# Performance work log

Measured on AMD Instinct MI355X. Metric: run time of the kernel, lower is better.

Reference implementation:

```python
import jax, jax.numpy as jnp
import numpy as np

B, H, W, C, NH, WS, SS = 32, 56, 56, 128, 4, 7, 3
L = H * W
N = WS * WS
HD = C // NH
EPS = 1e-5


def _rel_pos_index():
    coords = np.stack(np.meshgrid(np.arange(WS), np.arange(WS), indexing='ij'))  # (2,ws,ws)
    flat = coords.reshape(2, -1)  # (2,N)
    rel = flat[:, :, None] - flat[:, None, :]  # (2,N,N)
    rel = rel.transpose(1, 2, 0).astype(np.int64)
    rel[..., 0] += WS - 1
    rel[..., 1] += WS - 1
    rel[..., 0] *= 2 * WS - 1
    return jnp.asarray(rel.sum(-1), dtype=jnp.int32)  # (N,N)


def setup_inputs() -> dict:
    key = jax.random.key(0)
    ks = jax.random.split(key, 8)
    s = 0.02
    return {
        'x': jax.random.normal(ks[0], (B, L, C), jnp.float32),
        'norm1_g': jnp.ones((C,), jnp.float32),
        'norm1_b': jnp.zeros((C,), jnp.float32),
        'qkv_w': jax.random.normal(ks[1], (3 * C, C), jnp.float32) * s,
        'qkv_b': jnp.zeros((3 * C,), jnp.float32),
        'rpb_table': jax.random.normal(ks[2], ((2 * WS - 1) ** 2, NH), jnp.float32) * s,
        'proj_w': jax.random.normal(ks[3], (C, C), jnp.float32) * s,
        'proj_b': jnp.zeros((C,), jnp.float32),
        'norm2_g': jnp.ones((C,), jnp.float32),
        'norm2_b': jnp.zeros((C,), jnp.float32),
        'fc1_w': jax.random.normal(ks[4], (4 * C, C), jnp.float32) * s,
        'fc1_b': jnp.zeros((4 * C,), jnp.float32),
        'fc2_w': jax.random.normal(ks[5], (C, 4 * C), jnp.float32) * s,
        'fc2_b': jnp.zeros((C,), jnp.float32),
        'rel_idx': _rel_pos_index(),
    }


def _ln(h, g, b):
    mu = jnp.mean(h, axis=-1, keepdims=True)
    var = jnp.mean((h - mu) ** 2, axis=-1, keepdims=True)
    return (h - mu) * jax.lax.rsqrt(var + EPS) * g + b


def reference(x, norm1_g, norm1_b, qkv_w, qkv_b, rpb_table, proj_w, proj_b,
              norm2_g, norm2_b, fc1_w, fc1_b, fc2_w, fc2_b, rel_idx):
    nHw, nWw = H // WS, W // WS
    scale = HD ** (-0.5)

    shortcut = x
    h = _ln(x, norm1_g, norm1_b).reshape(B, H, W, C)
    # cyclic shift
    h = jnp.roll(h, shift=(-SS, -SS), axis=(1, 2))
    # window partition -> (B*nW, N, C)
    w = h.reshape(B, nHw, WS, nWw, WS, C).transpose(0, 1, 3, 2, 4, 5)
    w = w.reshape(B * nHw * nWw, N, C)

    qkv = w @ qkv_w.T + qkv_b  # (Bw, N, 3C)
    q, k, v = jnp.split(qkv, 3, axis=-1)
    q = q.reshape(-1, N, NH, HD).transpose(0, 2, 1, 3)  # (Bw, nh, N, hd)
    k = k.reshape(-1, N, NH, HD).transpose(0, 2, 1, 3)
    v = v.reshape(-1, N, NH, HD).transpose(0, 2, 1, 3)

    attn = jnp.einsum('bhnd,bhmd->bhnm', q * scale, k)
    bias = rpb_table[rel_idx.reshape(-1)].reshape(N, N, NH).transpose(2, 0, 1)  # (nh,N,N)
    attn = jax.nn.softmax(attn + bias[None], axis=-1)

    out = jnp.einsum('bhnm,bhmd->bhnd', attn, v)
    out = out.transpose(0, 2, 1, 3).reshape(-1, N, C)
    out = out @ proj_w.T + proj_b

    # window reverse + un-shift
    out = out.reshape(B, nHw, nWw, WS, WS, C).transpose(0, 1, 3, 2, 4, 5)
    out = out.reshape(B, H, W, C)
    out = jnp.roll(out, shift=(SS, SS), axis=(1, 2)).reshape(B, L, C)

    x = shortcut + out
    h2 = _ln(x, norm2_g, norm2_b)
    mlp = jax.nn.gelu(h2 @ fc1_w.T + fc1_b, approximate=False) @ fc2_w.T + fc2_b
    return x + mlp
```

## Files before the change

kernel.cpp:

```cpp
#include <hip/hip_runtime.h>

typedef unsigned short ushort_t;
typedef unsigned int uint_t;

typedef __bf16 bf16x8 __attribute__((ext_vector_type(8)));
typedef float f32x4 __attribute__((ext_vector_type(4)));

static __device__ __forceinline__ float bf2f(ushort_t h) {
    return __uint_as_float(((uint_t)h) << 16);
}
static __device__ __forceinline__ ushort_t f2bf(float f) {
    uint_t u = __float_as_uint(f);
    u = u + 0x7FFFu + ((u >> 16) & 1u);
    return (ushort_t)(u >> 16);
}
static __device__ __forceinline__ uint_t pkbf(float lo, float hi) {
    uint_t a = __float_as_uint(lo) + 0x8000u;
    uint_t b = __float_as_uint(hi) + 0x8000u;
    return __builtin_amdgcn_perm(b, a, 0x07060302u);
}

#define BB 32
#define HH 56
#define WW_ 56
#define CC 128
#define NHEAD 4
#define WS 7
#define SS 3
#define LL (HH * WW_)
#define NTOK (BB * LL)
#define NWIN (BB * 64)
#define NN 49
#define HD 32
#define QKS 32
#define PLS 40
#define VTS 72

static __device__ __forceinline__ int win2tok(int wid) {
    int win = wid / NN, t = wid - win * NN;
    int bb = win >> 6, wrem = win & 63;
    int wi = wrem >> 3, wj = wrem & 7;
    int ti = t / WS, tj = t - ti * WS;
    int hh = wi * WS + ti + SS; if (hh >= HH) hh -= HH;
    int ww = wj * WS + tj + SS; if (ww >= WW_) ww -= WW_;
    return bb * LL + hh * WW_ + ww;
}

__global__ __launch_bounds__(256) void prep_weights(
    const float* __restrict__ qkv_w, const float* __restrict__ proj_w,
    const float* __restrict__ fc1_w, const float* __restrict__ fc2_w,
    ushort_t* __restrict__ dst) {
    int i = blockIdx.x * 256 + threadIdx.x;
    const float* src;
    int off;
    if (i < 49152)        { src = qkv_w;  off = i; }
    else if (i < 65536)   { src = proj_w; off = i - 49152; }
    else if (i < 131072)  { src = fc1_w;  off = i - 65536; }
    else                  { src = fc2_w;  off = i - 131072; }
    dst[i] = f2bf(src[off]);
}

__global__ __launch_bounds__(256) void build_bias(
    const float* __restrict__ rpb, const int* __restrict__ rel_idx,
    float* __restrict__ bias) {
    int h = blockIdx.x;
    for (int idx = threadIdx.x; idx < 4096; idx += 256) {
        int i = idx >> 6, j = idx & 63;
        float v = 0.f;
        if (i < NN && j < NN)
            v = rpb[(size_t)rel_idx[i * NN + j] * NHEAD + h];
        bias[h * 4096 + idx] = v;
    }
}

__global__ __launch_bounds__(256) void win_block(
    const float* __restrict__ x, const float* __restrict__ g1,
    const float* __restrict__ b1, const ushort_t* __restrict__ wq,
    const float* __restrict__ qkv_b, const float* __restrict__ bias,
    ushort_t* __restrict__ attn_out, int win0) {
    __shared__ __align__(16) ushort_t U[16384];
    __shared__ __align__(16) ushort_t HV[NHEAD][32 * VTS];
    const int tid = threadIdx.x;
    const int wave = tid >> 6;
    const int lane = tid & 63;
    const int l16 = lane & 15;
    const int quad = lane >> 4;
    const int h = wave;
    const int win = win0 + blockIdx.x;
    const float scale = 0.17677669529663687f;

    ushort_t* XLN = U;
    ushort_t* QL = U + h * 4096;
    ushort_t* KL = QL + 2048;
    ushort_t* PL = QL;
    ushort_t* VT = HV[h];

    {
        int row = tid >> 2;
        int ch0 = (tid & 3) * 32;
        int t = (row < NN) ? row : 0;
        int gtok = win2tok(win * NN + t);
        const float* xp = x + (size_t)gtok * CC + ch0;
        float v[32];
        float s = 0.f, sq = 0.f;
        #pragma unroll
        for (int i = 0; i < 4; ++i) {
            float4 a0 = *(const float4*)(xp + i * 8);
            float4 a1 = *(const float4*)(xp + i * 8 + 4);
            v[i * 8 + 0] = a0.x; v[i * 8 + 1] = a0.y;
            v[i * 8 + 2] = a0.z; v[i * 8 + 3] = a0.w;
            v[i * 8 + 4] = a1.x; v[i * 8 + 5] = a1.y;
            v[i * 8 + 6] = a1.z; v[i * 8 + 7] = a1.w;
            #pragma unroll
            for (int j = 0; j < 8; ++j) { s += v[i * 8 + j]; sq += v[i * 8 + j] * v[i * 8 + j]; }
        }
        s += __shfl_xor(s, 1);  sq += __shfl_xor(sq, 1);
        s += __shfl_xor(s, 2);  sq += __shfl_xor(sq, 2);
        float mean = s * (1.0f / 128.0f);
        float var = sq * (1.0f / 128.0f) - mean * mean;
        float rstd = rsqrtf(var + 1e-5f);
        #pragma unroll
        for (int i = 0; i < 4; ++i) {
            ushort_t tmp[8];
            #pragma unroll
            for (int j = 0; j < 8; ++j) {
                int c = ch0 + i * 8 + j;
                tmp[j] = f2bf((v[i * 8 + j] - mean) * rstd * g1[c] + b1[c]);
            }
            *(uint4*)&XLN[row * 136 + ch0 + i * 8] = *(const uint4*)tmp;
        }
    }
    __syncthreads();

    bf16x8 tf[4][4];
    #pragma unroll
    for (int kk = 0; kk < 4; ++kk)
        #pragma unroll
        for (int i = 0; i < 4; ++i)
            tf[kk][i] = *(const bf16x8*)&XLN[(16 * i + l16) * 136 + kk * 32 + quad * 8];
    __syncthreads();

    {
        f32x4 s1[2][4];
        #pragma unroll
        for (int j = 0; j < 2; ++j)
            #pragma unroll
            for (int i = 0; i < 4; ++i)
                s1[j][i] = (f32x4){0.f, 0.f, 0.f, 0.f};
        #pragma unroll
        for (int kk = 0; kk < 4; ++kk)
            #pragma unroll
            for (int j = 0; j < 2; ++j) {
                bf16x8 wf = *(const bf16x8*)&wq[(size_t)(h * 32 + 16 * j + l16) * 128 + kk * 32 + quad * 8];
                #pragma unroll
                for (int i = 0; i < 4; ++i)
                    s1[j][i] = __builtin_amdgcn_mfma_f32_16x16x32_bf16(wf, tf[kk][i], s1[j][i], 0, 0, 0);
            }
        #pragma unroll
        for (int j = 0; j < 2; ++j) {
            float4 bv = *(const float4*)&qkv_b[h * 32 + 16 * j + quad * 4];
            #pragma unroll
            for (int i = 0; i < 4; ++i) {
                uint2 pk;
                pk.x = pkbf((s1[j][i][0] + bv.x) * scale, (s1[j][i][1] + bv.y) * scale);
                pk.y = pkbf((s1[j][i][2] + bv.z) * scale, (s1[j][i][3] + bv.w) * scale);
                *(uint2*)&QL[(16 * i + l16) * QKS + 16 * j + quad * 4] = pk;
            }
        }
    }
    {
        f32x4 s1[2][4];
        #pragma unroll
        for (int j = 0; j < 2; ++j)
            #pragma unroll
            for (int i = 0; i < 4; ++i)
                s1[j][i] = (f32x4){0.f, 0.f, 0.f, 0.f};
        #pragma unroll
        for (int kk = 0; kk < 4; ++kk)
            #pragma unroll
            for (int j = 0; j < 2; ++j) {
                bf16x8 wf = *(const bf16x8*)&wq[(size_t)(128 + h * 32 + 16 * j + l16) * 128 + kk * 32 + quad * 8];
                #pragma unroll
                for (int i = 0; i < 4; ++i)
                    s1[j][i] = __builtin_amdgcn_mfma_f32_16x16x32_bf16(wf, tf[kk][i], s1[j][i], 0, 0, 0);
            }
        #pragma unroll
        for (int j = 0; j < 2; ++j) {
            float4 bv = *(const float4*)&qkv_b[128 + h * 32 + 16 * j + quad * 4];
            #pragma unroll
            for (int i = 0; i < 4; ++i) {
                uint2 pk;
                pk.x = pkbf(s1[j][i][0] + bv.x, s1[j][i][1] + bv.y);
                pk.y = pkbf(s1[j][i][2] + bv.z, s1[j][i][3] + bv.w);
                *(uint2*)&KL[(16 * i + l16) * QKS + 16 * j + quad * 4] = pk;
            }
        }
    }
    {
        f32x4 sv[4][2];
        #pragma unroll
        for (int i = 0; i < 4; ++i)
            #pragma unroll
            for (int j = 0; j < 2; ++j)
                sv[i][j] = (f32x4){0.f, 0.f, 0.f, 0.f};
        #pragma unroll
        for (int kk = 0; kk < 4; ++kk)
            #pragma unroll
            for (int j = 0; j < 2; ++j) {
                bf16x8 wf = *(const bf16x8*)&wq[(size_t)(256 + h * 32 + 16 * j + l16) * 128 + kk * 32 + quad * 8];
                #pragma unroll
                for (int i = 0; i < 4; ++i)
                    sv[i][j] = __builtin_amdgcn_mfma_f32_16x16x32_bf16(tf[kk][i], wf, sv[i][j], 0, 0, 0);
            }
        #pragma unroll
        for (int j = 0; j < 2; ++j) {
            float bvv = qkv_b[256 + h * 32 + 16 * j + l16];
            #pragma unroll
            for (int i = 0; i < 4; ++i) {
                uint2 pk;
                pk.x = pkbf(sv[i][j][0] + bvv, sv[i][j][1] + bvv);
                pk.y = pkbf(sv[i][j][2] + bvv, sv[i][j][3] + bvv);
                *(uint2*)&VT[(16 * j + l16) * VTS + 16 * i + quad * 4] = pk;
            }
        }
    }

    f32x4 s[4][4];
    {
        bf16x8 qa[4], kb[4];
        #pragma unroll
        for (int t = 0; t < 4; ++t) {
            qa[t] = *(const bf16x8*)&QL[(16 * t + l16) * QKS + quad * 8];
            kb[t] = *(const bf16x8*)&KL[(16 * t + l16) * QKS + quad * 8];
        }
        #pragma unroll
        for (int mi = 0; mi < 4; ++mi)
            #pragma unroll
            for (int ni = 0; ni < 4; ++ni) {
                f32x4 z = {0.f, 0.f, 0.f, 0.f};
                s[mi][ni] = __builtin_amdgcn_mfma_f32_16x16x32_bf16(qa[mi], kb[ni], z, 0, 0, 0);
            }
    }

    const float* bh = bias + h * 4096;
    #pragma unroll
    for (int mi = 0; mi < 4; ++mi)
        #pragma unroll
        for (int ni = 0; ni < 4; ++ni)
            #pragma unroll
            for (int r = 0; r < 4; ++r)
                s[mi][ni][r] += bh[(16 * mi + quad * 4 + r) * 64 + 16 * ni + l16];

    #pragma unroll
    for (int mi = 0; mi < 4; ++mi)
        #pragma unroll
        for (int r = 0; r < 4; ++r) {
            float m01 = fmaxf(s[mi][0][r], s[mi][1][r]);
            float m2 = s[mi][2][r];
            float m3 = (l16 == 0) ? s[mi][3][r] : -3.0e38f;
            float mx = fmaxf(fmaxf(m01, m2), m3);
            mx = fmaxf(mx, __shfl_xor(mx, 1));
            mx = fmaxf(mx, __shfl_xor(mx, 2));
            mx = fmaxf(mx, __shfl_xor(mx, 4));
            mx = fmaxf(mx, __shfl_xor(mx, 8));
            float e0 = expf(s[mi][0][r] - mx);
            float e1 = expf(s[mi][1][r] - mx);
            float e2 = expf(s[mi][2][r] - mx);
            float e3 = (l16 == 0) ? expf(s[mi][3][r] - mx) : 0.f;
            float sum = (e0 + e1) + (e2 + e3);
            sum += __shfl_xor(sum, 1);
            sum += __shfl_xor(sum, 2);
            sum += __shfl_xor(sum, 4);
            sum += __shfl_xor(sum, 8);
            float inv = 1.0f / sum;
            s[mi][0][r] = e0 * inv;
            s[mi][1][r] = e1 * inv;
            s[mi][2][r] = e2 * inv;
            s[mi][3][r] = e3 * inv;
        }

    f32x4 o[2][4];
    #pragma unroll
    for (int it = 0; it < 2; ++it)
        #pragma unroll
        for (int jt = 0; jt < 4; ++jt)
            o[it][jt] = (f32x4){0.f, 0.f, 0.f, 0.f};
    #pragma unroll
    for (int k0 = 0; k0 < 64; k0 += 32) {
        int nb = k0 >> 4;
        #pragma unroll
        for (int mi = 0; mi < 4; ++mi)
            #pragma unroll
            for (int nn = 0; nn < 2; ++nn)
                #pragma unroll
                for (int r = 0; r < 4; ++r)
                    PL[(16 * mi + quad * 4 + r) * PLS + 16 * nn + l16] = f2bf(s[mi][nb + nn][r]);
        bf16x8 va[2], pb[4];
        #pragma unroll
        for (int it = 0; it < 2; ++it)
            va[it] = *(const bf16x8*)&VT[(16 * it + l16) * VTS + k0 + quad * 8];
        #pragma unroll
        for (int jt = 0; jt < 4; ++jt)
            pb[jt] = *(const bf16x8*)&PL[(16 * jt + l16) * PLS + quad * 8];
        #pragma unroll
        for (int it = 0; it < 2; ++it)
            #pragma unroll
            for (int jt = 0; jt < 4; ++jt)
                o[it][jt] = __builtin_amdgcn_mfma_f32_16x16x32_bf16(va[it], pb[jt], o[it][jt], 0, 0, 0);
    }

    #pragma unroll
    for (int jt = 0; jt < 4; ++jt) {
        int m = 16 * jt + l16;
        if (m < NN) {
            #pragma unroll
            for (int it = 0; it < 2; ++it) {
                ushort4 st;
                st.x = f2bf(o[it][jt][0]);
                st.y = f2bf(o[it][jt][1]);
                st.z = f2bf(o[it][jt][2]);
                st.w = f2bf(o[it][jt][3]);
                *(ushort4*)&attn_out[((size_t)(blockIdx.x * NN + m)) * CC + h * HD + 16 * it + quad * 4] = st;
            }
        }
    }
}

__global__ __launch_bounds__(256) void proj_mlp(
    const ushort_t* __restrict__ attn, const ushort_t* __restrict__ wp,
    const float* __restrict__ proj_b, const float* __restrict__ x,
    const float* __restrict__ g2, const float* __restrict__ b2,
    const ushort_t* __restrict__ w1, const float* __restrict__ b1,
    const ushort_t* __restrict__ w2, const float* __restrict__ bias2,
    float* __restrict__ out, int wid0) {
    __shared__ __align__(16) ushort_t AH[64 * 136];
    __shared__ __align__(16) ushort_t PS0[64 * 136];
    __shared__ __align__(16) ushort_t PS1[64 * 136];
    __shared__ float MRm[64];
    __shared__ float MRs[64];
    const int tid = threadIdx.x;
    const int m0 = blockIdx.x * 64;
    const int wave = tid >> 6;
    const int lane = tid & 63;
    const int l16 = lane & 15;
    const int quad = lane >> 4;
    const int wn = wave * 32;

    #pragma unroll
    for (int u = tid; u < 1024; u += 256) {
        int row = u >> 4, ch = (u & 15) * 8;
        *(uint4*)&AH[row * 136 + ch] = *(const uint4*)&attn[(size_t)(m0 + row) * CC + ch];
    }
    __syncthreads();

    {
        f32x4 pa[2][4];
        #pragma unroll
        for (int j = 0; j < 2; ++j)
            #pragma unroll
            for (int i = 0; i < 4; ++i)
                pa[j][i] = (f32x4){0.f, 0.f, 0.f, 0.f};
        #pragma unroll
        for (int kk = 0; kk < 4; ++kk) {
            bf16x8 tf[4];
            #pragma unroll
            for (int i = 0; i < 4; ++i)
                tf[i] = *(const bf16x8*)&AH[(16 * i + l16) * 136 + kk * 32 + quad * 8];
            #pragma unroll
            for (int j = 0; j < 2; ++j) {
                bf16x8 wf = *(const bf16x8*)&wp[(size_t)(wn + 16 * j + l16) * 128 + kk * 32 + quad * 8];
                #pragma unroll
                for (int i = 0; i < 4; ++i)
                    pa[j][i] = __builtin_amdgcn_mfma_f32_16x16x32_bf16(wf, tf[i], pa[j][i], 0, 0, 0);
            }
        }
        #pragma unroll
        for (int j = 0; j < 2; ++j) {
            float4 bv = *(const float4*)&proj_b[wn + 16 * j + quad * 4];
            #pragma unroll
            for (int i = 0; i < 4; ++i) {
                uint2 pk;
                pk.x = pkbf(pa[j][i][0] + bv.x, pa[j][i][1] + bv.y);
                pk.y = pkbf(pa[j][i][2] + bv.z, pa[j][i][3] + bv.w);
                *(uint2*)&PS0[(16 * i + l16) * 136 + wn + 16 * j + quad * 4] = pk;
            }
        }
    }
    __syncthreads();

    {
        int row = tid >> 2;
        int ch0 = (tid & 3) * 32;
        int gtok = win2tok(wid0 + m0 + row);
        const float* xp = x + (size_t)gtok * CC + ch0;
        float v[32];
        float s = 0.f, sq = 0.f;
        #pragma unroll
        for (int i = 0; i < 4; ++i) {
            float4 a0 = *(const float4*)(xp + i * 8);
            float4 a1 = *(const float4*)(xp + i * 8 + 4);
            ushort4 p0 = *(const ushort4*)&PS0[row * 136 + ch0 + i * 8];
            ushort4 p1 = *(const ushort4*)&PS0[row * 136 + ch0 + i * 8 + 4];
            v[i * 8 + 0] = a0.x + bf2f(p0.x); v[i * 8 + 1] = a0.y + bf2f(p0.y);
            v[i * 8 + 2] = a0.z + bf2f(p0.z); v[i * 8 + 3] = a0.w + bf2f(p0.w);
            v[i * 8 + 4] = a1.x + bf2f(p1.x); v[i * 8 + 5] = a1.y + bf2f(p1.y);
            v[i * 8 + 6] = a1.z + bf2f(p1.z); v[i * 8 + 7] = a1.w + bf2f(p1.w);
            #pragma unroll
            for (int j = 0; j < 8; ++j) { s += v[i * 8 + j]; sq += v[i * 8 + j] * v[i * 8 + j]; }
        }
        s += __shfl_xor(s, 1);  sq += __shfl_xor(sq, 1);
        s += __shfl_xor(s, 2);  sq += __shfl_xor(sq, 2);
        float mean = s * (1.0f / 128.0f);
        float var = sq * (1.0f / 128.0f) - mean * mean;
        float rstd = rsqrtf(var + 1e-5f);
        if ((tid & 3) == 0) {
            MRm[row] = mean;
            MRs[row] = (var + 1e-5f) * rstd;
        }
        #pragma unroll
        for (int i = 0; i < 4; ++i) {
            ushort_t tmp[8];
            #pragma unroll
            for (int j = 0; j < 8; ++j) {
                int c = ch0 + i * 8 + j;
                tmp[j] = f2bf((v[i * 8 + j] - mean) * rstd * g2[c] + b2[c]);
            }
            *(uint4*)&AH[row * 136 + ch0 + i * 8] = *(const uint4*)tmp;
        }
    }
    __syncthreads();

    f32x4 acc2[2][4];
    #pragma unroll
    for (int j = 0; j < 2; ++j)
        #pragma unroll
        for (int i = 0; i < 4; ++i)
            acc2[j][i] = (f32x4){0.f, 0.f, 0.f, 0.f};

    for (int c = 0; c < 4; ++c) {
        ushort_t* PB = (c & 1) ? PS1 : PS0;
        f32x4 s1[2][4];
        #pragma unroll
        for (int j = 0; j < 2; ++j)
            #pragma unroll
            for (int i = 0; i < 4; ++i)
                s1[j][i] = (f32x4){0.f, 0.f, 0.f, 0.f};
        #pragma unroll
        for (int kk = 0; kk < 4; ++kk) {
            bf16x8 tf[4];
            #pragma unroll
            for (int i = 0; i < 4; ++i)
                tf[i] = *(const bf16x8*)&AH[(16 * i + l16) * 136 + kk * 32 + quad * 8];
            #pragma unroll
            for (int j = 0; j < 2; ++j) {
                bf16x8 wf = *(const bf16x8*)&w1[(size_t)(c * 128 + wn + 16 * j + l16) * 128 + kk * 32 + quad * 8];
                #pragma unroll
                for (int i = 0; i < 4; ++i)
                    s1[j][i] = __builtin_amdgcn_mfma_f32_16x16x32_bf16(wf, tf[i], s1[j][i], 0, 0, 0);
            }
        }
        #pragma unroll
        for (int j = 0; j < 2; ++j) {
            float4 bv = *(const float4*)&b1[c * 128 + wn + 16 * j + quad * 4];
            #pragma unroll
            for (int i = 0; i < 4; ++i) {
                float g[4];
                #pragma unroll
                for (int r = 0; r < 4; ++r) {
                    float u = s1[j][i][r] + ((const float*)&bv)[r];
                    float z = 1.5957691216f * u * (1.0f + 0.044715f * u * u);
                    g[r] = u / (1.0f + __expf(-z));
                }
                uint2 pk;
                pk.x = pkbf(g[0], g[1]);
                pk.y = pkbf(g[2], g[3]);
                *(uint2*)&PB[(16 * i + l16) * 136 + wn + 16 * j + quad * 4] = pk;
            }
        }
        __syncthreads();
        #pragma unroll
        for (int kk = 0; kk < 4; ++kk) {
            bf16x8 pf[4];
            #pragma unroll
            for (int i = 0; i < 4; ++i)
                pf[i] = *(const bf16x8*)&PB[(16 * i + l16) * 136 + kk * 32 + quad * 8];
            #pragma unroll
            for (int j = 0; j < 2; ++j) {
                bf16x8 wf = *(const bf16x8*)&w2[(size_t)(wn + 16 * j + l16) * 512 + c * 128 + kk * 32 + quad * 8];
                #pragma unroll
                for (int i = 0; i < 4; ++i)
                    acc2[j][i] = __builtin_amdgcn_mfma_f32_16x16x32_bf16(wf, pf[i], acc2[j][i], 0, 0, 0);
            }
        }
    }

    int gt[4];
    #pragma unroll
    for (int i = 0; i < 4; ++i)
        gt[i] = win2tok(wid0 + m0 + 16 * i + l16);
    float invg[2][4], b2v[2][4];
    #pragma unroll
    for (int j = 0; j < 2; ++j) {
        float4 gv = *(const float4*)&g2[wn + 16 * j + quad * 4];
        float4 bv = *(const float4*)&b2[wn + 16 * j + quad * 4];
        invg[j][0] = 1.0f / gv.x; invg[j][1] = 1.0f / gv.y;
        invg[j][2] = 1.0f / gv.z; invg[j][3] = 1.0f / gv.w;
        b2v[j][0] = bv.x; b2v[j][1] = bv.y; b2v[j][2] = bv.z; b2v[j][3] = bv.w;
    }
    #pragma unroll
    for (int j = 0; j < 2; ++j) {
        float4 bb = *(const float4*)&bias2[wn + 16 * j + quad * 4];
        #pragma unroll
        for (int i = 0; i < 4; ++i) {
            int row = 16 * i + l16;
            float mean = MRm[row];
            float sd = MRs[row];
            ushort4 hv = *(const ushort4*)&AH[row * 136 + wn + 16 * j + quad * 4];
            float4 cur;
            cur.x = (bf2f(hv.x) - b2v[j][0]) * (invg[j][0] * sd) + mean + acc2[j][i][0] + bb.x;
            cur.y = (bf2f(hv.y) - b2v[j][1]) * (invg[j][1] * sd) + mean + acc2[j][i][1] + bb.y;
            cur.z = (bf2f(hv.z) - b2v[j][2]) * (invg[j][2] * sd) + mean + acc2[j][i][2] + bb.z;
            cur.w = (bf2f(hv.w) - b2v[j][3]) * (invg[j][3] * sd) + mean + acc2[j][i][3] + bb.w;
            *(float4*)(out + (size_t)gt[i] * CC + wn + 16 * j + quad * 4) = cur;
        }
    }
}

extern "C" void kernel_launch(void* const* d_in, const int* in_sizes, int n_in,
                              void* d_out, int out_size, void* d_ws, size_t ws_size,
                              hipStream_t stream) {
    const float* x       = (const float*)d_in[0];
    const float* norm1_g = (const float*)d_in[1];
    const float* norm1_b = (const float*)d_in[2];
    const float* qkv_w   = (const float*)d_in[3];
    const float* qkv_b   = (const float*)d_in[4];
    const float* rpb     = (const float*)d_in[5];
    const float* proj_w  = (const float*)d_in[6];
    const float* proj_b  = (const float*)d_in[7];
    const float* norm2_g = (const float*)d_in[8];
    const float* norm2_b = (const float*)d_in[9];
    const float* fc1_w   = (const float*)d_in[10];
    const float* fc1_b   = (const float*)d_in[11];
    const float* fc2_w   = (const float*)d_in[12];
    const float* fc2_b   = (const float*)d_in[13];
    const int*   rel_idx = (const int*)d_in[14];

    char* ws = (char*)d_ws;
    float*    biasT = (float*)ws;
    ushort_t* wall  = (ushort_t*)(ws + 65536);
    ushort_t* wqkv  = wall;
    ushort_t* wproj = wall + 49152;
    ushort_t* wfc1  = wall + 65536;
    ushort_t* wfc2  = wall + 131072;
    const size_t base = 524288;
    int f = 1;
    while (f < 16) {
        size_t szA = (size_t)NTOK * CC * 2 / f;
        if (base + szA <= ws_size) break;
        f *= 2;
    }
    int Mc = NTOK / f;
    int wc = NWIN / f;

    ushort_t* Areg = (ushort_t*)(ws + base);

    prep_weights<<<dim3(768), dim3(256), 0, stream>>>(qkv_w, proj_w, fc1_w, fc2_w, wall);
    build_bias<<<dim3(NHEAD), dim3(256), 0, stream>>>(rpb, rel_idx, biasT);
    for (int c = 0; c < f; ++c) {
        win_block<<<dim3(wc), dim3(256), 0, stream>>>(
            x, norm1_g, norm1_b, wqkv, qkv_b, biasT, Areg, c * wc);
        proj_mlp<<<dim3(Mc / 64), dim3(256), 0, stream>>>(
            Areg, wproj, proj_b, x, norm2_g, norm2_b,
            wfc1, fc1_b, wfc2, fc2_b, (float*)d_out, c * Mc);
    }
}
```

Measured before the change: 307.3 us.

## Fuse window attention and proj+MLP into one per-window kernel

Merges the attention kernel and the projection/LayerNorm/MLP kernel into a single kernel with one block per 7x7 window. Attention output stays in shared memory instead of round-tripping through a bf16 global buffer, and the chunked multi-launch loop goes away. In exchange, each 64-row tile now holds only 49 valid tokens, so the proj/MLP GEMMs do padded work. The single MLP staging buffer also needs extra barriers per chunk where the old code double-buffered.

```diff
diff --git a/kernel.cpp b/kernel.cpp
--- a/kernel.cpp
+++ b/kernel.cpp
@@ -73,20 +73,27 @@
     }
 }
 
-__global__ __launch_bounds__(256) void win_block(
+__global__ __launch_bounds__(256) void swin_fused(
     const float* __restrict__ x, const float* __restrict__ g1,
-    const float* __restrict__ b1, const ushort_t* __restrict__ wq,
+    const float* __restrict__ b1ln, const ushort_t* __restrict__ wq,
     const float* __restrict__ qkv_b, const float* __restrict__ bias,
-    ushort_t* __restrict__ attn_out, int win0) {
+    const ushort_t* __restrict__ wp, const float* __restrict__ proj_b,
+    const float* __restrict__ g2, const float* __restrict__ b2,
+    const ushort_t* __restrict__ w1, const float* __restrict__ fc1b,
+    const ushort_t* __restrict__ w2, const float* __restrict__ bias2,
+    float* __restrict__ out) {
     __shared__ __align__(16) ushort_t U[16384];
     __shared__ __align__(16) ushort_t HV[NHEAD][32 * VTS];
+    __shared__ float MRm[64];
+    __shared__ float MRs[64];
     const int tid = threadIdx.x;
     const int wave = tid >> 6;
     const int lane = tid & 63;
     const int l16 = lane & 15;
     const int quad = lane >> 4;
     const int h = wave;
-    const int win = win0 + blockIdx.x;
+    const int win = blockIdx.x;
+    const int wn = wave * 32;
     const float scale = 0.17677669529663687f;
 
     ushort_t* XLN = U;
@@ -94,6 +101,8 @@
     ushort_t* KL = QL + 2048;
     ushort_t* PL = QL;
     ushort_t* VT = HV[h];
+    ushort_t* AH = U;
+    ushort_t* PS = (ushort_t*)HV;
 
     {
         int row = tid >> 2;
@@ -125,7 +134,7 @@
             #pragma unroll
             for (int j = 0; j < 8; ++j) {
                 int c = ch0 + i * 8 + j;
-                tmp[j] = f2bf((v[i * 8 + j] - mean) * rstd * g1[c] + b1[c]);
+                tmp[j] = f2bf((v[i * 8 + j] - mean) * rstd * g1[c] + b1ln[c]);
             }
             *(uint4*)&XLN[row * 136 + ch0 + i * 8] = *(const uint4*)tmp;
         }
@@ -308,48 +317,20 @@
             for (int jt = 0; jt < 4; ++jt)
                 o[it][jt] = __builtin_amdgcn_mfma_f32_16x16x32_bf16(va[it], pb[jt], o[it][jt], 0, 0, 0);
     }
+    __syncthreads();
 
     #pragma unroll
     for (int jt = 0; jt < 4; ++jt) {
         int m = 16 * jt + l16;
-        if (m < NN) {
-            #pragma unroll
-            for (int it = 0; it < 2; ++it) {
-                ushort4 st;
-                st.x = f2bf(o[it][jt][0]);
-                st.y = f2bf(o[it][jt][1]);
-                st.z = f2bf(o[it][jt][2]);
-                st.w = f2bf(o[it][jt][3]);
-                *(ushort4*)&attn_out[((size_t)(blockIdx.x * NN + m)) * CC + h * HD + 16 * it + quad * 4] = st;
-            }
-        }
-    }
-}
-
-__global__ __launch_bounds__(256) void proj_mlp(
-    const ushort_t* __restrict__ attn, const ushort_t* __restrict__ wp,
-    const float* __restrict__ proj_b, const float* __restrict__ x,
-    const float* __restrict__ g2, const float* __restrict__ b2,
-    const ushort_t* __restrict__ w1, const float* __restrict__ b1,
-    const ushort_t* __restrict__ w2, const float* __restrict__ bias2,
-    float* __restrict__ out, int wid0) {
-    __shared__ __align__(16) ushort_t AH[64 * 136];
-    __shared__ __align__(16) ushort_t PS0[64 * 136];
-    __shared__ __align__(16) ushort_t PS1[64 * 136];
-    __shared__ float MRm[64];
-    __shared__ float MRs[64];
-    const int tid = threadIdx.x;
-    const int m0 = blockIdx.x * 64;
-    const int wave = tid >> 6;
-    const int lane = tid & 63;
-    const int l16 = lane & 15;
-    const int quad = lane >> 4;
-    const int wn = wave * 32;
-
-    #pragma unroll
-    for (int u = tid; u < 1024; u += 256) {
-        int row = u >> 4, ch = (u & 15) * 8;
-        *(uint4*)&AH[row * 136 + ch] = *(const uint4*)&attn[(size_t)(m0 + row) * CC + ch];
+        #pragma unroll
+        for (int it = 0; it < 2; ++it) {
+            ushort4 st;
+            st.x = f2bf(o[it][jt][0]);
+            st.y = f2bf(o[it][jt][1]);
+            st.z = f2bf(o[it][jt][2]);
+            st.w = f2bf(o[it][jt][3]);
+            *(ushort4*)&AH[m * 136 + h * HD + 16 * it + quad * 4] = st;
+        }
     }
     __syncthreads();
 
@@ -362,16 +343,16 @@
                 pa[j][i] = (f32x4){0.f, 0.f, 0.f, 0.f};
         #pragma unroll
         for (int kk = 0; kk < 4; ++kk) {
-            bf16x8 tf[4];
-            #pragma unroll
-            for (int i = 0; i < 4; ++i)
-                tf[i] = *(const bf16x8*)&AH[(16 * i + l16) * 136 + kk * 32 + quad * 8];
+            bf16x8 af[4];
+            #pragma unroll
+            for (int i = 0; i < 4; ++i)
+                af[i] = *(const bf16x8*)&AH[(16 * i + l16) * 136 + kk * 32 + quad * 8];
             #pragma unroll
             for (int j = 0; j < 2; ++j) {
                 bf16x8 wf = *(const bf16x8*)&wp[(size_t)(wn + 16 * j + l16) * 128 + kk * 32 + quad * 8];
                 #pragma unroll
                 for (int i = 0; i < 4; ++i)
-                    pa[j][i] = __builtin_amdgcn_mfma_f32_16x16x32_bf16(wf, tf[i], pa[j][i], 0, 0, 0);
+                    pa[j][i] = __builtin_amdgcn_mfma_f32_16x16x32_bf16(wf, af[i], pa[j][i], 0, 0, 0);
             }
         }
         #pragma unroll
@@ -382,7 +363,7 @@
                 uint2 pk;
                 pk.x = pkbf(pa[j][i][0] + bv.x, pa[j][i][1] + bv.y);
                 pk.y = pkbf(pa[j][i][2] + bv.z, pa[j][i][3] + bv.w);
-                *(uint2*)&PS0[(16 * i + l16) * 136 + wn + 16 * j + quad * 4] = pk;
+                *(uint2*)&PS[(16 * i + l16) * 136 + wn + 16 * j + quad * 4] = pk;
             }
         }
     }
@@ -391,26 +372,27 @@
     {
         int row = tid >> 2;
         int ch0 = (tid & 3) * 32;
-        int gtok = win2tok(wid0 + m0 + row);
+        int t = (row < NN) ? row : 0;
+        int gtok = win2tok(win * NN + t);
         const float* xp = x + (size_t)gtok * CC + ch0;
         float v[32];
-        float s = 0.f, sq = 0.f;
+        float s2 = 0.f, sq = 0.f;
         #pragma unroll
         for (int i = 0; i < 4; ++i) {
             float4 a0 = *(const float4*)(xp + i * 8);
             float4 a1 = *(const float4*)(xp + i * 8 + 4);
-            ushort4 p0 = *(const ushort4*)&PS0[row * 136 + ch0 + i * 8];
-            ushort4 p1 = *(const ushort4*)&PS0[row * 136 + ch0 + i * 8 + 4];
+            ushort4 p0 = *(const ushort4*)&PS[row * 136 + ch0 + i * 8];
+            ushort4 p1 = *(const ushort4*)&PS[row * 136 + ch0 + i * 8 + 4];
             v[i * 8 + 0] = a0.x + bf2f(p0.x); v[i * 8 + 1] = a0.y + bf2f(p0.y);
             v[i * 8 + 2] = a0.z + bf2f(p0.z); v[i * 8 + 3] = a0.w + bf2f(p0.w);
             v[i * 8 + 4] = a1.x + bf2f(p1.x); v[i * 8 + 5] = a1.y + bf2f(p1.y);
             v[i * 8 + 6] = a1.z + bf2f(p1.z); v[i * 8 + 7] = a1.w + bf2f(p1.w);
             #pragma unroll
-            for (int j = 0; j < 8; ++j) { s += v[i * 8 + j]; sq += v[i * 8 + j] * v[i * 8 + j]; }
-        }
-        s += __shfl_xor(s, 1);  sq += __shfl_xor(sq, 1);
-        s += __shfl_xor(s, 2);  sq += __shfl_xor(sq, 2);
-        float mean = s * (1.0f / 128.0f);
+            for (int j = 0; j < 8; ++j) { s2 += v[i * 8 + j]; sq += v[i * 8 + j] * v[i * 8 + j]; }
+        }
+        s2 += __shfl_xor(s2, 1);  sq += __shfl_xor(sq, 1);
+        s2 += __shfl_xor(s2, 2);  sq += __shfl_xor(sq, 2);
+        float mean = s2 * (1.0f / 128.0f);
         float var = sq * (1.0f / 128.0f) - mean * mean;
         float rstd = rsqrtf(var + 1e-5f);
         if ((tid & 3) == 0) {
@@ -438,7 +420,6 @@
             acc2[j][i] = (f32x4){0.f, 0.f, 0.f, 0.f};
 
     for (int c = 0; c < 4; ++c) {
-        ushort_t* PB = (c & 1) ? PS1 : PS0;
         f32x4 s1[2][4];
         #pragma unroll
         for (int j = 0; j < 2; ++j)
@@ -447,21 +428,22 @@
                 s1[j][i] = (f32x4){0.f, 0.f, 0.f, 0.f};
         #pragma unroll
         for (int kk = 0; kk < 4; ++kk) {
-            bf16x8 tf[4];
-            #pragma unroll
-            for (int i = 0; i < 4; ++i)
-                tf[i] = *(const bf16x8*)&AH[(16 * i + l16) * 136 + kk * 32 + quad * 8];
+            bf16x8 hf[4];
+            #pragma unroll
+            for (int i = 0; i < 4; ++i)
+                hf[i] = *(const bf16x8*)&AH[(16 * i + l16) * 136 + kk * 32 + quad * 8];
             #pragma unroll
             for (int j = 0; j < 2; ++j) {
                 bf16x8 wf = *(const bf16x8*)&w1[(size_t)(c * 128 + wn + 16 * j + l16) * 128 + kk * 32 + quad * 8];
                 #pragma unroll
                 for (int i = 0; i < 4; ++i)
-                    s1[j][i] = __builtin_amdgcn_mfma_f32_16x16x32_bf16(wf, tf[i], s1[j][i], 0, 0, 0);
-            }
-        }
+                    s1[j][i] = __builtin_amdgcn_mfma_f32_16x16x32_bf16(wf, hf[i], s1[j][i], 0, 0, 0);
+            }
+        }
+        uint2 pk[2][4];
         #pragma unroll
         for (int j = 0; j < 2; ++j) {
-            float4 bv = *(const float4*)&b1[c * 128 + wn + 16 * j + quad * 4];
+            float4 bv = *(const float4*)&fc1b[c * 128 + wn + 16 * j + quad * 4];
             #pragma unroll
             for (int i = 0; i < 4; ++i) {
                 float g[4];
@@ -471,19 +453,23 @@
                     float z = 1.5957691216f * u * (1.0f + 0.044715f * u * u);
                     g[r] = u / (1.0f + __expf(-z));
                 }
-                uint2 pk;
-                pk.x = pkbf(g[0], g[1]);
-                pk.y = pkbf(g[2], g[3]);
-                *(uint2*)&PB[(16 * i + l16) * 136 + wn + 16 * j + quad * 4] = pk;
-            }
-        }
+                pk[j][i].x = pkbf(g[0], g[1]);
+                pk[j][i].y = pkbf(g[2], g[3]);
+            }
+        }
+        __syncthreads();
+        #pragma unroll
+        for (int j = 0; j < 2; ++j)
+            #pragma unroll
+            for (int i = 0; i < 4; ++i)
+                *(uint2*)&PS[(16 * i + l16) * 136 + wn + 16 * j + quad * 4] = pk[j][i];
         __syncthreads();
         #pragma unroll
         for (int kk = 0; kk < 4; ++kk) {
             bf16x8 pf[4];
             #pragma unroll
             for (int i = 0; i < 4; ++i)
-                pf[i] = *(const bf16x8*)&PB[(16 * i + l16) * 136 + kk * 32 + quad * 8];
+                pf[i] = *(const bf16x8*)&PS[(16 * i + l16) * 136 + kk * 32 + quad * 8];
             #pragma unroll
             for (int j = 0; j < 2; ++j) {
                 bf16x8 wf = *(const bf16x8*)&w2[(size_t)(wn + 16 * j + l16) * 512 + c * 128 + kk * 32 + quad * 8];
@@ -494,10 +480,6 @@
         }
     }
 
-    int gt[4];
-    #pragma unroll
-    for (int i = 0; i < 4; ++i)
-        gt[i] = win2tok(wid0 + m0 + 16 * i + l16);
     float invg[2][4], b2v[2][4];
     #pragma unroll
     for (int j = 0; j < 2; ++j) {
@@ -508,20 +490,23 @@
         b2v[j][0] = bv.x; b2v[j][1] = bv.y; b2v[j][2] = bv.z; b2v[j][3] = bv.w;
     }
     #pragma unroll
-    for (int j = 0; j < 2; ++j) {
-        float4 bb = *(const float4*)&bias2[wn + 16 * j + quad * 4];
-        #pragma unroll
-        for (int i = 0; i < 4; ++i) {
-            int row = 16 * i + l16;
+    for (int i = 0; i < 4; ++i) {
+        int row = 16 * i + l16;
+        if (row < NN) {
+            int gtok = win2tok(win * NN + row);
             float mean = MRm[row];
             float sd = MRs[row];
-            ushort4 hv = *(const ushort4*)&AH[row * 136 + wn + 16 * j + quad * 4];
-            float4 cur;
-            cur.x = (bf2f(hv.x) - b2v[j][0]) * (invg[j][0] * sd) + mean + acc2[j][i][0] + bb.x;
-            cur.y = (bf2f(hv.y) - b2v[j][1]) * (invg[j][1] * sd) + mean + acc2[j][i][1] + bb.y;
-            cur.z = (bf2f(hv.z) - b2v[j][2]) * (invg[j][2] * sd) + mean + acc2[j][i][2] + bb.z;
-            cur.w = (bf2f(hv.w) - b2v[j][3]) * (invg[j][3] * sd) + mean + acc2[j][i][3] + bb.w;
-            *(float4*)(out + (size_t)gt[i] * CC + wn + 16 * j + quad * 4) = cur;
+            #pragma unroll
+            for (int j = 0; j < 2; ++j) {
+                float4 bb = *(const float4*)&bias2[wn + 16 * j + quad * 4];
+                ushort4 hv = *(const ushort4*)&AH[row * 136 + wn + 16 * j + quad * 4];
+                float4 cur;
+                cur.x = (bf2f(hv.x) - b2v[j][0]) * (invg[j][0] * sd) + mean + acc2[j][i][0] + bb.x;
+                cur.y = (bf2f(hv.y) - b2v[j][1]) * (invg[j][1] * sd) + mean + acc2[j][i][1] + bb.y;
+                cur.z = (bf2f(hv.z) - b2v[j][2]) * (invg[j][2] * sd) + mean + acc2[j][i][2] + bb.z;
+                cur.w = (bf2f(hv.w) - b2v[j][3]) * (invg[j][3] * sd) + mean + acc2[j][i][3] + bb.w;
+                *(float4*)(out + (size_t)gtok * CC + wn + 16 * j + quad * 4) = cur;
+            }
         }
     }
 }
@@ -552,25 +537,11 @@
     ushort_t* wproj = wall + 49152;
     ushort_t* wfc1  = wall + 65536;
     ushort_t* wfc2  = wall + 131072;
-    const size_t base = 524288;
-    int f = 1;
-    while (f < 16) {
-        size_t szA = (size_t)NTOK * CC * 2 / f;
-        if (base + szA <= ws_size) break;
-        f *= 2;
-    }
-    int Mc = NTOK / f;
-    int wc = NWIN / f;
-
-    ushort_t* Areg = (ushort_t*)(ws + base);
 
     prep_weights<<<dim3(768), dim3(256), 0, stream>>>(qkv_w, proj_w, fc1_w, fc2_w, wall);
     build_bias<<<dim3(NHEAD), dim3(256), 0, stream>>>(rpb, rel_idx, biasT);
-    for (int c = 0; c < f; ++c) {
-        win_block<<<dim3(wc), dim3(256), 0, stream>>>(
-            x, norm1_g, norm1_b, wqkv, qkv_b, biasT, Areg, c * wc);
-        proj_mlp<<<dim3(Mc / 64), dim3(256), 0, stream>>>(
-            Areg, wproj, proj_b, x, norm2_g, norm2_b,
-            wfc1, fc1_b, wfc2, fc2_b, (float*)d_out, c * Mc);
-    }
-}
+    swin_fused<<<dim3(NWIN), dim3(256), 0, stream>>>(
+        x, norm1_g, norm1_b, wqkv, qkv_b, biasT,
+        wproj, proj_b, norm2_g, norm2_b,
+        wfc1, fc1_b, wfc2, fc2_b, (float*)d_out);
+}
```

Result: no change. 307.9 us (+0.2%).
